# Optimization experiments

Hardware: AMD Instinct MI355X
Metric: run time of the kernel (lower is better)

The kernel has to match this reference:

```python
import jax, jax.numpy as jnp
import numpy as np

BATCH, SEQ, DMODEL, DHID = 4, 4096, 1024, 1024
R_MIN, R_MAX = 0.9, 0.99
MAX_PHASE = np.pi / 50  # module overrides ctor arg with pi/50
EPS = 1e-5


def setup_inputs() -> dict:
    key = jax.random.key(0)
    ks = jax.random.split(key, 8)
    # nu_init
    u1 = jax.random.uniform(ks[0], (DHID,)) * (1 - EPS) + EPS
    mag_sq = u1 * (R_MAX ** 2 - R_MIN ** 2) + R_MIN ** 2
    nu_log = jnp.log(-0.5 * jnp.log(mag_sq + EPS))
    # theta_init
    u2 = jax.random.uniform(ks[1], (DHID,)) * (1 - EPS) + EPS
    theta_log = jnp.log(MAX_PHASE * u2)
    B_re = jax.random.normal(ks[2], (DHID, DMODEL)) / np.sqrt(2 * DMODEL)
    B_im = jax.random.normal(ks[3], (DHID, DMODEL)) / np.sqrt(2 * DMODEL)
    C_re = jax.random.normal(ks[4], (DMODEL, DHID)) / np.sqrt(DHID)
    C_im = jax.random.normal(ks[5], (DMODEL, DHID)) / np.sqrt(DHID)
    D_skip = jax.random.normal(ks[6], (DMODEL,))
    inputs = jax.random.normal(ks[7], (BATCH, SEQ, DMODEL), dtype=jnp.float32)
    return {"inputs": inputs, "nu_log": nu_log, "theta_log": theta_log,
            "B_re": B_re, "B_im": B_im, "C_re": C_re, "C_im": C_im,
            "D_skip": D_skip}


def reference(inputs, nu_log, theta_log, B_re, B_im, C_re, C_im, D_skip):
    nu = jnp.exp(nu_log)
    theta = jnp.exp(theta_log)
    diag_lambda = jnp.exp(-nu + 1j * theta)            # [H] complex
    # forward recomputes gamma_log from nu_log (parameter gamma_log unused)
    gamma_log = 0.5 * jnp.log(1 - jnp.exp(-2 * jnp.exp(nu_log)) + EPS)
    B_norm = (B_re + 1j * B_im) * jnp.exp(gamma_log)[:, None]  # [H, D]
    inputs_c = inputs.astype(jnp.complex64)
    Bu = jnp.einsum('hd,btd->bth', B_norm, inputs_c)   # [B, T, H]

    def step(h, bu_t):
        h = diag_lambda * h + bu_t
        return h, h

    h0 = jnp.zeros((inputs.shape[0], diag_lambda.shape[0]), dtype=Bu.dtype)
    _, hs = jax.lax.scan(step, h0, jnp.swapaxes(Bu, 0, 1))  # [T, B, H]
    hs = jnp.swapaxes(hs, 0, 1)                              # [B, T, H]
    C_complex = C_re + 1j * C_im                              # [D, H]
    out = jnp.einsum('bth,dh->btd', hs, C_complex).real + inputs * D_skip
    return out.astype(jnp.float32)
```

## Files before the change

kernel.cpp:

```cpp
#include <hip/hip_runtime.h>


typedef __bf16 bf16x8 __attribute__((ext_vector_type(8)));
typedef float floatx4 __attribute__((ext_vector_type(4)));

__device__ __forceinline__ unsigned short f2bf(float f) {
  unsigned u = __float_as_uint(f);
  u += 0x7fffu + ((u >> 16) & 1u);
  return (unsigned short)(u >> 16);
}
__device__ __forceinline__ float bf2f(unsigned short s) {
  return __uint_as_float(((unsigned)s) << 16);
}


__global__ void prep_params(const float* __restrict__ nu_log,
                            const float* __restrict__ theta_log,
                            float* __restrict__ lam,
                            float* __restrict__ lamL,
                            float* __restrict__ gamma)
{
  int h = blockIdx.x * 256 + threadIdx.x;
  float nu = expf(nu_log[h]);
  float th = expf(theta_log[h]);
  float r = expf(-nu);
  lam[h]        = r * cosf(th);
  lam[1024 + h] = r * sinf(th);
  float rL = expf(-128.0f * nu);
  lamL[h]        = rL * cosf(128.0f * th);
  lamL[1024 + h] = rL * sinf(128.0f * th);
  gamma[h] = sqrtf(1.0f - expf(-2.0f * nu) + 1e-5f);
}

__global__ void prep_B(const float* __restrict__ B_re, const float* __restrict__ B_im,
                       const float* __restrict__ gamma, unsigned short* __restrict__ Bcat)
{
  int tid = blockIdx.x * 256 + threadIdx.x;
  int n = tid >> 10;
  int d = tid & 1023;
  int h = n & 1023;
  float v = (n < 1024 ? B_re[h * 1024 + d] : B_im[h * 1024 + d]) * gamma[h];
  Bcat[tid] = f2bf(v);
}

__global__ void prep_C(const float* __restrict__ C_re, const float* __restrict__ C_im,
                       unsigned short* __restrict__ Ccat)
{
  int tid = blockIdx.x * 256 + threadIdx.x;
  int d = tid >> 11;
  int k = tid & 2047;
  float v = (k < 1024) ? C_re[d * 1024 + k] : -C_im[d * 1024 + (k - 1024)];
  Ccat[tid] = f2bf(v);
}

__global__ void conv_inputs(const float* __restrict__ in, unsigned short* __restrict__ outb)
{
  int tid = blockIdx.x * 256 + threadIdx.x;
  float4 v = ((const float4*)in)[tid];
  unsigned lo = (unsigned)f2bf(v.x) | ((unsigned)f2bf(v.y) << 16);
  unsigned hi = (unsigned)f2bf(v.z) | ((unsigned)f2bf(v.w) << 16);
  ((uint2*)outb)[tid] = make_uint2(lo, hi);
}


#define GLDS(gp, lp) __builtin_amdgcn_global_load_lds(                        \
      (const __attribute__((address_space(1))) void*)(gp),                    \
      (__attribute__((address_space(3))) void*)(lp), 16, 0, 0)

#define STAGE(kt, buf) do {                                                   \
    const int _ko = (kt) * 32;                                                \
    GLDS(gA0 + _ko, &As[(buf)][lofs0]);                                       \
    GLDS(gA1 + _ko, &As[(buf)][lofs1]);                                       \
    GLDS(gB0 + _ko, &Bs[(buf)][lofs0]);                                       \
    GLDS(gB1 + _ko, &Bs[(buf)][lofs1]);                                       \
  } while (0)

#define READ_B(buf) do {                                                      \
    _Pragma("unroll")                                                         \
    for (int j = 0; j < 4; ++j) {                                             \
      const int r = wn * 64 + j * 16 + lm;                                    \
      bfr[j] = *reinterpret_cast<const bf16x8*>(                              \
          &Bs[(buf)][r * 32 + (q ^ ((r >> 1) & 3)) * 8]);                     \
    }                                                                         \
  } while (0)

#define READ_A(buf, i0) do {                                                  \
    _Pragma("unroll")                                                         \
    for (int i = 0; i < 4; ++i) {                                             \
      const int r = wm * 128 + ((i0) + i) * 16 + lm;                          \
      afr[i] = *reinterpret_cast<const bf16x8*>(                              \
          &As[(buf)][r * 32 + (q ^ ((r >> 1) & 3)) * 8]);                     \
    }                                                                         \
  } while (0)

#define MFMA16(i0) do {                                                       \
    __builtin_amdgcn_s_setprio(1);                                            \
    _Pragma("unroll")                                                         \
    for (int i = 0; i < 4; ++i)                                               \
      _Pragma("unroll")                                                       \
      for (int j = 0; j < 4; ++j)                                             \
        acc[(i0) + i][j] = __builtin_amdgcn_mfma_f32_16x16x32_bf16(           \
            afr[i], bfr[j], acc[(i0) + i][j], 0, 0, 0);                       \
    __builtin_amdgcn_s_setprio(0);                                            \
  } while (0)

#define BAR() do {                                                            \
    __builtin_amdgcn_sched_barrier(0);                                        \
    asm volatile("" ::: "memory");                                            \
    __builtin_amdgcn_s_barrier();                                             \
    asm volatile("" ::: "memory");                                            \
    __builtin_amdgcn_sched_barrier(0);                                        \
  } while (0)

template <int EPI>
__global__ __launch_bounds__(512, 2) void gemm256_kernel(
    const unsigned short* __restrict__ A,
    const unsigned short* __restrict__ Bt,
    void* __restrict__ Cout,
    int M, int N, int K,
    const float* __restrict__ skip_in,
    const float* __restrict__ skip_w)
{
  __shared__ __align__(16) unsigned short As[4][256 * 32];
  __shared__ __align__(16) unsigned short Bs[4][256 * 32];

  const int tid  = threadIdx.x;
  const int lane = tid & 63;
  const int wave = tid >> 6;
  const int wm = wave >> 2;
  const int wn = wave & 3;

  const int flat    = blockIdx.x;
  const int xcd     = flat & 7;
  const int local   = flat >> 3;
  const int m_tile  = xcd * 8 + (local & 7);
  const int n_tile  = local >> 3;
  const int m0 = m_tile * 256;
  const int n0 = n_tile * 256;

  const int ldr = lane >> 2;
  const int pos = lane & 3;
  const int lm  = lane & 15;
  const int q   = lane >> 4;

  const int r0 = wave * 32 + ldr;
  const int r1 = r0 + 16;
  const int ca0 = pos ^ ((r0 >> 1) & 3);
  const int ca1 = pos ^ ((r1 >> 1) & 3);

  const unsigned short* gA0 = A  + (size_t)(m0 + r0) * K + ca0 * 8;
  const unsigned short* gA1 = A  + (size_t)(m0 + r1) * K + ca1 * 8;
  const unsigned short* gB0 = Bt + (size_t)(n0 + r0) * K + ca0 * 8;
  const unsigned short* gB1 = Bt + (size_t)(n0 + r1) * K + ca1 * 8;
  const int lofs0 = r0 * 32 + pos * 8;
  const int lofs1 = r1 * 32 + pos * 8;

  floatx4 acc[8][4];
#pragma unroll
  for (int i = 0; i < 8; ++i)
#pragma unroll
    for (int j = 0; j < 4; ++j)
      acc[i][j] = (floatx4){0.f, 0.f, 0.f, 0.f};

  const int KT = K >> 5;

  STAGE(0, 0);
  STAGE(1, 1);
  STAGE(2, 2);
  asm volatile("s_waitcnt vmcnt(8)" ::: "memory");
  __builtin_amdgcn_s_barrier();
  asm volatile("" ::: "memory");

  for (int kt = 0; kt + 3 < KT; ++kt) {
    const int cur = kt & 3;
    const int b3  = (kt + 3) & 3;
    const int ko3 = (kt + 3) * 32;
    bf16x8 afr[4], bfr[4];

    READ_B(cur);
    READ_A(cur, 0);
    GLDS(gA0 + ko3, &As[b3][lofs0]);
    GLDS(gA1 + ko3, &As[b3][lofs1]);
    BAR();
    MFMA16(0);
    BAR();

    READ_A(cur, 4);
    GLDS(gB0 + ko3, &Bs[b3][lofs0]);
    GLDS(gB1 + ko3, &Bs[b3][lofs1]);
    asm volatile("s_waitcnt vmcnt(8)" ::: "memory");
    BAR();
    MFMA16(4);
    BAR();
  }

  {
    const int cur = (KT - 3) & 3;
    bf16x8 afr[4], bfr[4];
    READ_B(cur);
    READ_A(cur, 0);
    BAR();
    MFMA16(0);
    BAR();
    READ_A(cur, 4);
    asm volatile("s_waitcnt vmcnt(4)" ::: "memory");
    BAR();
    MFMA16(4);
    BAR();
  }
  {
    const int cur = (KT - 2) & 3;
    bf16x8 afr[4], bfr[4];
    READ_B(cur);
    READ_A(cur, 0);
    BAR();
    MFMA16(0);
    BAR();
    READ_A(cur, 4);
    asm volatile("s_waitcnt vmcnt(0)" ::: "memory");
    BAR();
    MFMA16(4);
    BAR();
  }
  {
    const int cur = (KT - 1) & 3;
    bf16x8 afr[4], bfr[4];
    READ_B(cur);
    READ_A(cur, 0);
    MFMA16(0);
    READ_A(cur, 4);
    MFMA16(4);
  }

#pragma unroll
  for (int i = 0; i < 8; ++i) {
#pragma unroll
    for (int j = 0; j < 4; ++j) {
      const int row0 = m0 + wm * 128 + i * 16 + q * 4;
      const int col  = n0 + wn * 64 + j * 16 + lm;
#pragma unroll
      for (int r = 0; r < 4; ++r) {
        const size_t idx = (size_t)(row0 + r) * N + col;
        if (EPI == 0) {
          ((unsigned short*)Cout)[idx] = f2bf(acc[i][j][r]);
        } else {
          ((float*)Cout)[idx] = acc[i][j][r] + skip_in[idx] * skip_w[col];
        }
      }
    }
  }
}


__global__ void scan_finals(const unsigned short* __restrict__ Bu,
                            const float* __restrict__ lam,
                            float2* __restrict__ finals)
{
  int tid = blockIdx.x * 256 + threadIdx.x;
  int h = tid & 1023, c = (tid >> 10) & 31, b = tid >> 15;
  float lre = lam[h], lim = lam[1024 + h];
  const unsigned short* p = Bu + ((size_t)(b * 4096 + c * 128) * 2048) + h;
  float yre = 0.f, yim = 0.f;
#pragma unroll 4
  for (int t = 0; t < 128; ++t) {
    float ure = bf2f(p[0]);
    float uim = bf2f(p[1024]);
    float nre = fmaf(lre, yre, fmaf(-lim, yim, ure));
    float nim = fmaf(lre, yim, fmaf(lim, yre, uim));
    yre = nre; yim = nim;
    p += 2048;
  }
  finals[tid] = make_float2(yre, yim);
}

__global__ void scan_carries(const float2* __restrict__ finals,
                             const float* __restrict__ lamL,
                             float2* __restrict__ carry)
{
  int tid = blockIdx.x * 256 + threadIdx.x;
  int h = tid & 1023, b = tid >> 10;
  float Lre = lamL[h], Lim = lamL[1024 + h];
  float Hre = 0.f, Him = 0.f;
  for (int c = 0; c < 32; ++c) {
    size_t i = ((size_t)(b * 32 + c) << 10) + h;
    carry[i] = make_float2(Hre, Him);
    float2 f = finals[i];
    float nre = fmaf(Lre, Hre, fmaf(-Lim, Him, f.x));
    float nim = fmaf(Lre, Him, fmaf(Lim, Hre, f.y));
    Hre = nre; Him = nim;
  }
}

__global__ void scan_apply(const float* __restrict__ lam,
                           const float2* __restrict__ carry,
                           unsigned short* __restrict__ Bu)
{
  int tid = blockIdx.x * 256 + threadIdx.x;
  int h = tid & 1023, c = (tid >> 10) & 31, b = tid >> 15;
  float lre = lam[h], lim = lam[1024 + h];
  float2 cv = carry[tid];
  float yre = cv.x, yim = cv.y;
  unsigned short* p = Bu + ((size_t)(b * 4096 + c * 128) * 2048) + h;
#pragma unroll 4
  for (int t = 0; t < 128; ++t) {
    float ure = bf2f(p[0]);
    float uim = bf2f(p[1024]);
    float nre = fmaf(lre, yre, fmaf(-lim, yim, ure));
    float nim = fmaf(lre, yim, fmaf(lim, yre, uim));
    yre = nre; yim = nim;
    p[0]    = f2bf(yre);
    p[1024] = f2bf(yim);
    p += 2048;
  }
}


extern "C" void kernel_launch(void* const* d_in, const int* in_sizes, int n_in,
                              void* d_out, int out_size, void* d_ws, size_t ws_size,
                              hipStream_t stream)
{
  const float* inputs    = (const float*)d_in[0];
  const float* nu_log    = (const float*)d_in[1];
  const float* theta_log = (const float*)d_in[2];
  const float* B_re      = (const float*)d_in[3];
  const float* B_im      = (const float*)d_in[4];
  const float* C_re      = (const float*)d_in[5];
  const float* C_im      = (const float*)d_in[6];
  const float* D_skip    = (const float*)d_in[7];
  float* out = (float*)d_out;

  char* ws = (char*)d_ws;
  float* lam   = (float*)ws;
  float* lamL  = lam + 2048;
  float* gamma = lamL + 2048;
  unsigned short* inp_bf = (unsigned short*)(ws + (1 << 16));
  unsigned short* Bcat   = inp_bf + (size_t)16384 * 1024;
  unsigned short* Ccat   = Bcat   + (size_t)2048 * 1024;
  unsigned short* Bu     = Ccat   + (size_t)1024 * 2048;
  float2* finals = (float2*)(Bu + (size_t)16384 * 2048);
  float2* carry  = finals + 131072;

  prep_params<<<4,    256, 0, stream>>>(nu_log, theta_log, lam, lamL, gamma);
  prep_B     <<<8192, 256, 0, stream>>>(B_re, B_im, gamma, Bcat);
  prep_C     <<<8192, 256, 0, stream>>>(C_re, C_im, Ccat);
  conv_inputs<<<16384,256, 0, stream>>>(inputs, inp_bf);

  gemm256_kernel<0><<<512, 512, 0, stream>>>(
      inp_bf, Bcat, Bu, 16384, 2048, 1024, nullptr, nullptr);

  scan_finals <<<512, 256, 0, stream>>>(Bu, lam, finals);
  scan_carries<<<16,  256, 0, stream>>>(finals, lamL, carry);
  scan_apply  <<<512, 256, 0, stream>>>(lam, carry, Bu);

  gemm256_kernel<1><<<256, 512, 0, stream>>>(
      Bu, Ccat, out, 16384, 1024, 2048, inputs, D_skip);
}
```

Before: 330.1 us.

## Halve GEMM main-loop barriers and overlap second A-fragment reads with MFMAs

Expands the A-fragment register array to eight entries so the second half of A can be read from LDS while the first MFMA batch runs. It cuts the barriers per K-step from four to two: one pacing barrier, and one certifying barrier that waits on vmcnt and lgkmcnt before the second MFMA batch. This is meant to reduce barrier stalls and hide LDS read latency behind matrix math. The cost is higher VGPR pressure, which may hurt occupancy at 2 blocks per CU, and it relies on the reordered waits still protecting the 4-stage LDS ring from overwrites.

New measurement: 337.0 us. +2.1%, slower.

```diff
diff --git a/kernel.cpp b/kernel.cpp
--- a/kernel.cpp
+++ b/kernel.cpp
@@ -88,7 +88,7 @@
     _Pragma("unroll")                                                         \
     for (int i = 0; i < 4; ++i) {                                             \
       const int r = wm * 128 + ((i0) + i) * 16 + lm;                          \
-      afr[i] = *reinterpret_cast<const bf16x8*>(                              \
+      afr[(i0) + i] = *reinterpret_cast<const bf16x8*>(                       \
           &As[(buf)][r * 32 + (q ^ ((r >> 1) & 3)) * 8]);                     \
     }                                                                         \
   } while (0)
@@ -100,16 +100,28 @@
       _Pragma("unroll")                                                       \
       for (int j = 0; j < 4; ++j)                                             \
         acc[(i0) + i][j] = __builtin_amdgcn_mfma_f32_16x16x32_bf16(           \
-            afr[i], bfr[j], acc[(i0) + i][j], 0, 0, 0);                       \
+            afr[(i0) + i], bfr[j], acc[(i0) + i][j], 0, 0, 0);                \
     __builtin_amdgcn_s_setprio(0);                                            \
   } while (0)
 
-#define BAR() do {                                                            \
-    __builtin_amdgcn_sched_barrier(0);                                        \
+#define SB0() __builtin_amdgcn_sched_barrier(0)
+
+#define BAR_PACE() do {                                                       \
+    SB0();                                                                    \
     asm volatile("" ::: "memory");                                            \
     __builtin_amdgcn_s_barrier();                                             \
     asm volatile("" ::: "memory");                                            \
-    __builtin_amdgcn_sched_barrier(0);                                        \
+    SB0();                                                                    \
+  } while (0)
+
+#define BAR_CERT(vm) do {                                                     \
+    SB0();                                                                    \
+    asm volatile("s_waitcnt vmcnt(" #vm ")" ::: "memory");                    \
+    asm volatile("s_waitcnt lgkmcnt(0)" ::: "memory");                        \
+    SB0();                                                                    \
+    __builtin_amdgcn_s_barrier();                                             \
+    asm volatile("" ::: "memory");                                            \
+    SB0();                                                                    \
   } while (0)
 
 template <int EPI>
@@ -171,60 +183,48 @@
   __builtin_amdgcn_s_barrier();
   asm volatile("" ::: "memory");
 
+  bf16x8 afr[8], bfr[4];
+
   for (int kt = 0; kt + 3 < KT; ++kt) {
     const int cur = kt & 3;
     const int b3  = (kt + 3) & 3;
     const int ko3 = (kt + 3) * 32;
-    bf16x8 afr[4], bfr[4];
 
     READ_B(cur);
     READ_A(cur, 0);
     GLDS(gA0 + ko3, &As[b3][lofs0]);
     GLDS(gA1 + ko3, &As[b3][lofs1]);
-    BAR();
+    BAR_PACE();
+    READ_A(cur, 4);
     MFMA16(0);
-    BAR();
-
-    READ_A(cur, 4);
     GLDS(gB0 + ko3, &Bs[b3][lofs0]);
     GLDS(gB1 + ko3, &Bs[b3][lofs1]);
-    asm volatile("s_waitcnt vmcnt(8)" ::: "memory");
-    BAR();
+    BAR_CERT(8);
     MFMA16(4);
-    BAR();
   }
 
   {
     const int cur = (KT - 3) & 3;
-    bf16x8 afr[4], bfr[4];
     READ_B(cur);
     READ_A(cur, 0);
-    BAR();
+    BAR_PACE();
+    READ_A(cur, 4);
     MFMA16(0);
-    BAR();
-    READ_A(cur, 4);
-    asm volatile("s_waitcnt vmcnt(4)" ::: "memory");
-    BAR();
+    BAR_CERT(4);
     MFMA16(4);
-    BAR();
   }
   {
     const int cur = (KT - 2) & 3;
-    bf16x8 afr[4], bfr[4];
     READ_B(cur);
     READ_A(cur, 0);
-    BAR();
+    BAR_PACE();
+    READ_A(cur, 4);
     MFMA16(0);
-    BAR();
-    READ_A(cur, 4);
-    asm volatile("s_waitcnt vmcnt(0)" ::: "memory");
-    BAR();
+    BAR_CERT(0);
     MFMA16(4);
-    BAR();
   }
   {
     const int cur = (KT - 1) & 3;
-    bf16x8 afr[4], bfr[4];
     READ_B(cur);
     READ_A(cur, 0);
     MFMA16(0);
```
